# Optimization experiments

Hardware: AMD Instinct MI355X
Metric: run time of the kernel (lower is better)

The kernel has to match this reference:

```python
import jax, jax.numpy as jnp
import numpy as np

B_, H_, W_ = 4, 64, 64
D_MODEL, D_INNER, N_STATE, R_RANK, K_ = 96, 192, 16, 6, 4
EPS = 1e-5

def silu(v):
    return v * jax.nn.sigmoid(v)

def setup_inputs() -> dict:
    key = jax.random.key(0)
    ks = jax.random.split(key, 8)
    d, dm = D_INNER, D_MODEL
    A = jnp.tile(jnp.arange(1, N_STATE + 1, dtype=jnp.float32)[None, :], (K_ * d, 1))
    return {
        "x": jax.random.normal(ks[0], (B_, H_, W_, dm), jnp.float32),
        "in_proj_w": jax.random.normal(ks[1], (2 * d, dm), jnp.float32) * 0.02,
        "conv_w": jax.random.normal(ks[2], (d, 1, 3, 3), jnp.float32) * 0.1,
        "conv_b": jnp.zeros((d,), jnp.float32),
        "x_proj_weight": jax.random.normal(ks[3], (K_, R_RANK + 2 * N_STATE, d), jnp.float32) * 0.05,
        "dt_projs_weight": jax.random.normal(ks[4], (K_, d, R_RANK), jnp.float32) * 0.1,
        "dt_projs_bias": jax.random.normal(ks[5], (K_, d), jnp.float32) * 0.1,
        "A_logs": jnp.log(A),
        "Ds": jnp.ones((K_ * d,), jnp.float32),
        "out_norm_w": jnp.ones((d,), jnp.float32),
        "out_norm_b": jnp.zeros((d,), jnp.float32),
        "out_proj_w": jax.random.normal(ks[6], (dm, d), jnp.float32) * 0.02,
    }

def selective_scan(u, dts, As, Bs, Cs, Ds, dt_bias):
    # u, dts: [B,K,D,L]; As: [K,D,N]; Bs, Cs: [B,K,N,L]; Ds, dt_bias: [K,D]
    delta = jax.nn.softplus(dts + dt_bias[None, :, :, None])
    dT = jnp.moveaxis(delta, -1, 0)  # [L,B,K,D]
    uT = jnp.moveaxis(u, -1, 0)      # [L,B,K,D]
    BT = jnp.moveaxis(Bs, -1, 0)     # [L,B,K,N]
    CT = jnp.moveaxis(Cs, -1, 0)     # [L,B,K,N]
    h0 = jnp.zeros((u.shape[0], K_, D_INNER, N_STATE), jnp.float32)

    def step(h, inps):
        dt, ut, bt, ct = inps
        h = jnp.exp(dt[..., None] * As[None]) * h + (dt * ut)[..., None] * bt[:, :, None, :]
        y = jnp.einsum('bkdn,bkn->bkd', h, ct)
        return h, y

    _, ys = jax.lax.scan(step, h0, (dT, uT, BT, CT))
    ys = jnp.moveaxis(ys, 0, -1)  # [B,K,D,L]
    return ys + u * Ds[None, :, :, None]

def reference(x, in_proj_w, conv_w, conv_b, x_proj_weight, dt_projs_weight,
              dt_projs_bias, A_logs, Ds, out_norm_w, out_norm_b, out_proj_w):
    B, H, W, dm = x.shape
    d, N, R, K = D_INNER, N_STATE, R_RANK, K_
    L = H * W
    # in_proj + z gate (SiLU)
    xz = jnp.einsum('bhwc,pc->bhwp', x, in_proj_w)  # [B,H,W,2d]
    xc, z = xz[..., :d], xz[..., d:]
    z = silu(z)
    # depthwise conv (NCHW) + SiLU
    xc = jnp.transpose(xc, (0, 3, 1, 2))  # [B,d,H,W]
    xc = jax.lax.conv_general_dilated(
        xc, conv_w, (1, 1), 'SAME', feature_group_count=d,
        dimension_numbers=('NCHW', 'OIHW', 'NCHW')) + conv_b[None, :, None, None]
    xc = silu(xc)
    # cross-scan: 4 directions
    x0 = xc.reshape(B, d, L)                                   # row-major
    x1 = jnp.transpose(xc, (0, 1, 3, 2)).reshape(B, d, L)       # col-major
    xs = jnp.stack([x0, x1, x0[..., ::-1], x1[..., ::-1]], axis=1)  # [B,K,D,L]
    # projections
    x_dbl = jnp.einsum('bkdl,kcd->bkcl', xs, x_proj_weight)
    dts, Bs, Cs = jnp.split(x_dbl, [R, R + N], axis=2)
    dts = jnp.einsum('bkrl,kdr->bkdl', dts, dt_projs_weight)
    As = -jnp.exp(A_logs).reshape(K, d, N)
    ys = selective_scan(xs, dts, As, Bs, Cs, Ds.reshape(K, d), dt_projs_bias)
    # cross-merge
    y_wh = (ys[:, 1] + ys[:, 3, :, ::-1]).reshape(B, d, W, H)
    y_wh = jnp.transpose(y_wh, (0, 1, 3, 2)).reshape(B, d, L)
    y = ys[:, 0] + ys[:, 2, :, ::-1] + y_wh                     # [B,d,L]
    y = jnp.transpose(y.reshape(B, d, H, W), (0, 2, 3, 1))       # [B,H,W,d]
    # out_norm: LayerNorm over channel dim
    mu = jnp.mean(y, axis=-1, keepdims=True)
    var = jnp.mean((y - mu) ** 2, axis=-1, keepdims=True)
    y = out_norm_w * (y - mu) * jax.lax.rsqrt(var + EPS) + out_norm_b
    # gate + out_proj
    y = y * z
    return jnp.einsum('bhwd,cd->bhwc', y, out_proj_w)
```

## Files before the change

### kernel.cpp

```cpp
#include <hip/hip_runtime.h>
#include <math.h>

#define B_ 4
#define HH 64
#define WW 64
#define LL 4096
#define DM 96
#define DI 192
#define NS 16
#define RR 6
#define KK 4
#define NROW (B_ * KK * DI)
#define XPS 160
#define KOFF 40

__device__ __forceinline__ int pix_of(int k, int l) {
    switch (k) {
        case 0: return l;
        case 1: { int w = l >> 6, h = l & 63; return (h << 6) + w; }
        case 2: return (LL - 1) - l;
        default: { int ll = (LL - 1) - l; int w = ll >> 6, h = ll & 63; return (h << 6) + w; }
    }
}

__device__ __forceinline__ float silu_f(float v) {
    return v * __fdividef(1.f, 1.f + __expf(-v));
}
__device__ __forceinline__ float softplus_f(float x) {
    return (x > 20.f) ? x : __logf(1.f + __expf(x));
}

template<int MODE>
__global__ __launch_bounds__(256)
void gemm_kernel(const float* __restrict__ A, const float* __restrict__ Bw,
                 float* __restrict__ C0, float* __restrict__ C1,
                 int M, int N, int Kd) {
    __shared__ float As[32][68];
    __shared__ float Bs[32][68];
    int tid = threadIdx.x;
    int tx = tid & 15, ty = tid >> 4;
    int m0 = blockIdx.y * 64, n0 = blockIdx.x * 64;
    float acc[4][4] = {};
    for (int k0 = 0; k0 < Kd; k0 += 32) {
        #pragma unroll
        for (int i = 0; i < 8; ++i) {
            int idx = tid + i * 256;
            int r = idx >> 5, c = idx & 31;
            As[c][r] = A[(size_t)(m0 + r) * Kd + k0 + c];
            int rn = n0 + r;
            Bs[c][r] = (rn < N) ? Bw[(size_t)rn * Kd + k0 + c] : 0.f;
        }
        __syncthreads();
        #pragma unroll
        for (int kk = 0; kk < 32; ++kk) {
            float4 av = *(const float4*)&As[kk][ty * 4];
            float4 bv = *(const float4*)&Bs[kk][tx * 4];
            const float* avp = (const float*)&av;
            const float* bvp = (const float*)&bv;
            #pragma unroll
            for (int i = 0; i < 4; ++i)
                #pragma unroll
                for (int j = 0; j < 4; ++j)
                    acc[i][j] += avp[i] * bvp[j];
        }
        __syncthreads();
    }
    #pragma unroll
    for (int i = 0; i < 4; ++i) {
        int m = m0 + ty * 4 + i;
        #pragma unroll
        for (int j = 0; j < 4; ++j) {
            int n = n0 + tx * 4 + j;
            if (n >= N) continue;
            float v = acc[i][j];
            if (MODE == 0) {
                if (n < DI) C0[(size_t)m * DI + n] = v;
                else        C1[(size_t)m * DI + (n - DI)] = silu_f(v);
            } else if (MODE == 1) {
                C0[(size_t)m * N + n] = v;
            } else {
                if (n < 152) {
                    int kd = n / 38, c = n - kd * 38;
                    C0[(size_t)m * XPS + kd * KOFF + c] = v;
                }
            }
        }
    }
}

__global__ __launch_bounds__(192)
void conv_kernel(const float* __restrict__ xc, const float* __restrict__ cw,
                 const float* __restrict__ cb, float* __restrict__ out) {
    int p0 = blockIdx.x * 8;
    int b = blockIdx.y;
    int c = threadIdx.x;
    int h = p0 >> 6, w0 = p0 & 63;
    float kw[9];
    #pragma unroll
    for (int j = 0; j < 9; ++j) kw[j] = cw[c * 9 + j];
    float xv[3][10];
    #pragma unroll
    for (int dh = 0; dh < 3; ++dh) {
        int hh = h + dh - 1;
        bool hv = (hh >= 0 && hh < HH);
        #pragma unroll
        for (int j = 0; j < 10; ++j) {
            int ww = w0 + j - 1;
            bool v = hv && (ww >= 0 && ww < WW);
            xv[dh][j] = v ? xc[((size_t)(b << 12) + (hh << 6) + ww) * DI + c] : 0.f;
        }
    }
    float bias = cb[c];
    #pragma unroll
    for (int w = 0; w < 8; ++w) {
        float acc = bias;
        #pragma unroll
        for (int dh = 0; dh < 3; ++dh)
            #pragma unroll
            for (int dc = 0; dc < 3; ++dc)
                acc += xv[dh][w + dc] * kw[dh * 3 + dc];
        out[((size_t)(b << 12) + p0 + w) * DI + c] = silu_f(acc);
    }
}

template<int PHASE, int NCHT>
__global__ __launch_bounds__(192)
void scan_phase(const float* __restrict__ xconv, const float* __restrict__ xdblP,
                const float* __restrict__ dtw, const float* __restrict__ dtb,
                const float* __restrict__ A_logs, const float* __restrict__ Ds,
                float* __restrict__ carryA, float* __restrict__ carryB,
                float* __restrict__ y_acc) {
    constexpr int CHL = LL / NCHT;
    constexpr int NV4 = (PHASE == 3) ? (KOFF / 4) : 6;
    int chunk = blockIdx.x;
    int k = blockIdx.y;
    int b = blockIdx.z;
    int d = threadIdx.x;
    int l0 = chunk * CHL;
    __shared__ float sx[CHL * NV4 * 4];
    float4* sx4 = (float4*)sx;
    const float* xb = xdblP + ((size_t)(b << 12)) * XPS + k * KOFF;
    for (int idx = d; idx < CHL * NV4; idx += DI) {
        int r = idx / NV4, j = idx - r * NV4;
        int p = pix_of(k, l0 + r);
        sx4[idx] = *(const float4*)(xb + (size_t)p * XPS + j * 4);
    }

    float wr[RR];
    #pragma unroll
    for (int r = 0; r < RR; ++r) wr[r] = dtw[(k * DI + d) * RR + r];
    float bias = dtb[k * DI + d];
    const float* alog = A_logs + (size_t)(k * DI + d) * NS;
    bool fastA = true;
    #pragma unroll
    for (int n = 0; n < NS; ++n) {
        float an = -__expf(alog[n]);
        fastA = fastA && (fabsf(an + (float)(n + 1)) < 1e-4f * (float)(n + 1));
    }
    float h[NS];
    int row = (b * KK + k) * DI + d;
    if (PHASE == 1) {
        #pragma unroll
        for (int n = 0; n < NS; ++n) h[n] = 0.f;
    } else {
        #pragma unroll
        for (int n = 0; n < NS; ++n) h[n] = carryB[((size_t)chunk * NROW + row) * NS + n];
    }
    float Dk = (PHASE == 3) ? Ds[k * DI + d] : 0.f;
    float sumDelta = 0.f;
    const float* ubase = xconv + (size_t)(b << 12) * DI + d;
    float* ybase = y_acc + (size_t)(b << 12) * DI + d;
    __syncthreads();

    int p_cur = pix_of(k, l0);
    float u_cur = ubase[(size_t)p_cur * DI];
    for (int i = 0; i < CHL; ++i) {
        int p_nxt = 0; float u_nxt = 0.f;
        if (i + 1 < CHL) {
            p_nxt = pix_of(k, l0 + i + 1);
            u_nxt = ubase[(size_t)p_nxt * DI];
        }
        float xrv[NV4 * 4];
        float4* x4 = (float4*)xrv;
        #pragma unroll
        for (int j = 0; j < NV4; ++j) x4[j] = sx4[i * NV4 + j];
        float dtraw = bias;
        #pragma unroll
        for (int r = 0; r < RR; ++r) dtraw += xrv[r] * wr[r];
        float delta = softplus_f(dtraw);
        if (PHASE == 1) sumDelta += delta;
        float du = delta * u_cur;
        float y = 0.f;
        if (fastA) {
            float g = __expf(-delta);
            float a = 1.f;
            #pragma unroll
            for (int n = 0; n < NS; ++n) {
                a *= g;
                h[n] = a * h[n] + du * xrv[6 + n];
                if (PHASE == 3) y += h[n] * xrv[22 + n];
            }
        } else {
            #pragma unroll
            for (int n = 0; n < NS; ++n) {
                float a = __expf(delta * (-__expf(alog[n])));
                h[n] = a * h[n] + du * xrv[6 + n];
                if (PHASE == 3) y += h[n] * xrv[22 + n];
            }
        }
        if (PHASE == 3) {
            y += u_cur * Dk;
            atomicAdd(&ybase[(size_t)p_cur * DI], y);
        }
        p_cur = p_nxt;
        u_cur = u_nxt;
    }
    if (PHASE == 1) {
        #pragma unroll
        for (int n = 0; n < NS; ++n) {
            float An = -__expf(alog[n]);
            carryA[((size_t)chunk * NROW + row) * NS + n] = __expf(An * sumDelta);
            carryB[((size_t)chunk * NROW + row) * NS + n] = h[n];
        }
    }
}

template<int NCHT>
__global__ __launch_bounds__(256)
void scan_chunks(const float* __restrict__ carryA, float* __restrict__ carryB) {
    int t = blockIdx.x * 256 + threadIdx.x;
    if (t >= NROW * NS) return;
    float h = 0.f;
    for (int c = 0; c < NCHT; ++c) {
        size_t idx = (size_t)c * (NROW * NS) + t;
        float a = carryA[idx], bb = carryB[idx];
        carryB[idx] = h;
        h = a * h + bb;
    }
}

__global__ __launch_bounds__(256)
void ln_kernel(const float* __restrict__ y_acc, const float* __restrict__ z_silu,
               const float* __restrict__ nw, const float* __restrict__ nb,
               float* __restrict__ out) {
    int pg = blockIdx.x * 4 + (threadIdx.x >> 6);
    int lane = threadIdx.x & 63;
    const float* yr = y_acc + (size_t)pg * DI;
    float v0 = yr[lane], v1 = yr[lane + 64], v2 = yr[lane + 128];
    float s = v0 + v1 + v2;
    float sq = v0 * v0 + v1 * v1 + v2 * v2;
    #pragma unroll
    for (int m = 32; m >= 1; m >>= 1) {
        s  += __shfl_xor(s, m, 64);
        sq += __shfl_xor(sq, m, 64);
    }
    float mu = s * (1.f / 192.f);
    float var = sq * (1.f / 192.f) - mu * mu;
    float rs = rsqrtf(var + 1e-5f);
    const float* zr = z_silu + (size_t)pg * DI;
    float* o = out + (size_t)pg * DI;
    float vv[3] = {v0, v1, v2};
    #pragma unroll
    for (int j = 0; j < 3; ++j) {
        int c = lane + j * 64;
        o[c] = (nw[c] * (vv[j] - mu) * rs + nb[c]) * zr[c];
    }
}

extern "C" void kernel_launch(void* const* d_in, const int* in_sizes, int n_in,
                              void* d_out, int out_size, void* d_ws, size_t ws_size,
                              hipStream_t stream) {
    const float* x        = (const float*)d_in[0];
    const float* in_projw = (const float*)d_in[1];
    const float* conv_w   = (const float*)d_in[2];
    const float* conv_b   = (const float*)d_in[3];
    const float* x_projw  = (const float*)d_in[4];
    const float* dt_w     = (const float*)d_in[5];
    const float* dt_b     = (const float*)d_in[6];
    const float* A_logs   = (const float*)d_in[7];
    const float* Ds       = (const float*)d_in[8];
    const float* nw       = (const float*)d_in[9];
    const float* nb       = (const float*)d_in[10];
    const float* opw      = (const float*)d_in[11];
    float* out = (float*)d_out;
    float* ws = (float*)d_ws;

    const size_t SZ = (size_t)B_ * LL * DI;
    const size_t XD = (size_t)B_ * LL * XPS;

    const size_t car128 = (size_t)NROW * 128 * NS;
    const size_t need128 = (3 * SZ + XD + 2 * car128) * sizeof(float);
    bool big = (ws_size >= need128);

    float* z_silu = ws;
    float* xc_raw = ws + SZ;
    float* xconv  = ws + 2 * SZ;
    float* xdblP  = ws + 3 * SZ;
    float* carryA = ws + 3 * SZ + XD;
    float* carryB = carryA + (big ? car128 : (size_t)NROW * 64 * NS);
    float* y_acc  = xc_raw;
    float* yln    = xconv;

    gemm_kernel<0><<<dim3(6, 256), 256, 0, stream>>>(x, in_projw, xc_raw, z_silu,
                                                     B_ * LL, 2 * DI, DM);
    conv_kernel<<<dim3(LL / 8, B_), DI, 0, stream>>>(xc_raw, conv_w, conv_b, xconv);
    gemm_kernel<2><<<dim3(3, 256), 256, 0, stream>>>(xconv, x_projw, xdblP, nullptr,
                                                     B_ * LL, 152, DI);

    if (big) {
        scan_phase<1, 128><<<dim3(128, KK, B_), DI, 0, stream>>>(xconv, xdblP, dt_w, dt_b,
                                                                 A_logs, Ds, carryA, carryB, nullptr);
        scan_chunks<128><<<(NROW * NS + 255) / 256, 256, 0, stream>>>(carryA, carryB);
        hipMemsetAsync(y_acc, 0, SZ * sizeof(float), stream);
        scan_phase<3, 128><<<dim3(128, KK, B_), DI, 0, stream>>>(xconv, xdblP, dt_w, dt_b,
                                                                 A_logs, Ds, carryA, carryB, y_acc);
    } else {
        scan_phase<1, 64><<<dim3(64, KK, B_), DI, 0, stream>>>(xconv, xdblP, dt_w, dt_b,
                                                               A_logs, Ds, carryA, carryB, nullptr);
        scan_chunks<64><<<(NROW * NS + 255) / 256, 256, 0, stream>>>(carryA, carryB);
        hipMemsetAsync(y_acc, 0, SZ * sizeof(float), stream);
        scan_phase<3, 64><<<dim3(64, KK, B_), DI, 0, stream>>>(xconv, xdblP, dt_w, dt_b,
                                                               A_logs, Ds, carryA, carryB, y_acc);
    }
    ln_kernel<<<(B_ * LL) / 4, 256, 0, stream>>>(y_acc, z_silu, nw, nb, yln);
    gemm_kernel<1><<<dim3(2, 256), 256, 0, stream>>>(yln, opw, out, nullptr,
                                                     B_ * LL, DM, DI);
}
```

Before: 219.4 us.

## Derive scan decay from the softplus sigmoid and drop the carryA buffer

Rewrites the fast-A decay so that exp(-softplus(x)) comes from 1/(1+e^x), reusing the exp already computed for softplus. The per-state powers are built with a shallow multiplication tree instead of a serial chain, and the y reduction is split into four partial sums to shorten dependency chains. Pixel addressing uses a pointer stepped by a constant stride per direction. The carryA buffer is replaced by a per-row sum of delta, and scan_chunks now computes the chunk decay from that sum, which cuts carry traffic. The small-workspace fallback is removed and the last iteration prefetches one element past the chunk, so the code assumes a large enough workspace and tolerates that out-of-range read.

```diff
diff --git a/kernel.cpp b/kernel.cpp
--- a/kernel.cpp
+++ b/kernel.cpp
@@ -25,9 +25,6 @@
 
 __device__ __forceinline__ float silu_f(float v) {
     return v * __fdividef(1.f, 1.f + __expf(-v));
-}
-__device__ __forceinline__ float softplus_f(float x) {
-    return (x > 20.f) ? x : __logf(1.f + __expf(x));
 }
 
 template<int MODE>
@@ -128,7 +125,7 @@
 void scan_phase(const float* __restrict__ xconv, const float* __restrict__ xdblP,
                 const float* __restrict__ dtw, const float* __restrict__ dtb,
                 const float* __restrict__ A_logs, const float* __restrict__ Ds,
-                float* __restrict__ carryA, float* __restrict__ carryB,
+                float* __restrict__ sumD, float* __restrict__ carryB,
                 float* __restrict__ y_acc) {
     constexpr int CHL = LL / NCHT;
     constexpr int NV4 = (PHASE == 3) ? (KOFF / 4) : 6;
@@ -163,23 +160,27 @@
         #pragma unroll
         for (int n = 0; n < NS; ++n) h[n] = 0.f;
     } else {
-        #pragma unroll
-        for (int n = 0; n < NS; ++n) h[n] = carryB[((size_t)chunk * NROW + row) * NS + n];
+        const float4* cb4 = (const float4*)(carryB + ((size_t)chunk * NROW + row) * NS);
+        #pragma unroll
+        for (int q = 0; q < NS / 4; ++q) {
+            float4 v = cb4[q];
+            h[q * 4 + 0] = v.x; h[q * 4 + 1] = v.y;
+            h[q * 4 + 2] = v.z; h[q * 4 + 3] = v.w;
+        }
     }
     float Dk = (PHASE == 3) ? Ds[k * DI + d] : 0.f;
     float sumDelta = 0.f;
-    const float* ubase = xconv + (size_t)(b << 12) * DI + d;
-    float* ybase = y_acc + (size_t)(b << 12) * DI + d;
     __syncthreads();
 
-    int p_cur = pix_of(k, l0);
-    float u_cur = ubase[(size_t)p_cur * DI];
+    int s = (k == 0) ? 1 : (k == 1) ? 64 : (k == 2) ? -1 : -64;
+    int p0 = pix_of(k, l0);
+    intptr_t stp = (intptr_t)s * DI;
+    const float* up = xconv + (size_t)(b << 12) * DI + (size_t)p0 * DI + d;
+    float* yp = y_acc + (size_t)(b << 12) * DI + (size_t)p0 * DI + d;
+    float u_cur = *up;
+
     for (int i = 0; i < CHL; ++i) {
-        int p_nxt = 0; float u_nxt = 0.f;
-        if (i + 1 < CHL) {
-            p_nxt = pix_of(k, l0 + i + 1);
-            u_nxt = ubase[(size_t)p_nxt * DI];
-        }
+        float u_nxt = *(up + stp);
         float xrv[NV4 * 4];
         float4* x4 = (float4*)xrv;
         #pragma unroll
@@ -187,20 +188,27 @@
         float dtraw = bias;
         #pragma unroll
         for (int r = 0; r < RR; ++r) dtraw += xrv[r] * wr[r];
-        float delta = softplus_f(dtraw);
+        float e = __expf(dtraw);
+        float g = __fdividef(1.f, 1.f + e);
+        float delta = (dtraw > 20.f) ? dtraw : __logf(1.f + e);
         if (PHASE == 1) sumDelta += delta;
         float du = delta * u_cur;
-        float y = 0.f;
+        float y;
         if (fastA) {
-            float g = __expf(-delta);
-            float a = 1.f;
+            float a[NS];
+            a[0] = g;          a[1] = g * g;      a[2] = a[1] * g;    a[3] = a[1] * a[1];
+            a[4] = a[3] * g;   a[5] = a[3] * a[1]; a[6] = a[3] * a[2]; a[7] = a[3] * a[3];
+            a[8] = a[7] * g;   a[9] = a[7] * a[1]; a[10] = a[7] * a[2]; a[11] = a[7] * a[3];
+            a[12] = a[7] * a[4]; a[13] = a[7] * a[5]; a[14] = a[7] * a[6]; a[15] = a[7] * a[7];
+            float yp4[4] = {0.f, 0.f, 0.f, 0.f};
             #pragma unroll
             for (int n = 0; n < NS; ++n) {
-                a *= g;
-                h[n] = a * h[n] + du * xrv[6 + n];
-                if (PHASE == 3) y += h[n] * xrv[22 + n];
+                h[n] = a[n] * h[n] + du * xrv[6 + n];
+                if (PHASE == 3) yp4[n & 3] += h[n] * xrv[22 + n];
             }
+            y = (yp4[0] + yp4[1]) + (yp4[2] + yp4[3]);
         } else {
+            y = 0.f;
             #pragma unroll
             for (int n = 0; n < NS; ++n) {
                 float a = __expf(delta * (-__expf(alog[n])));
@@ -210,31 +218,40 @@
         }
         if (PHASE == 3) {
             y += u_cur * Dk;
-            atomicAdd(&ybase[(size_t)p_cur * DI], y);
-        }
-        p_cur = p_nxt;
+            atomicAdd(yp, y);
+            yp += stp;
+        }
+        up += stp;
         u_cur = u_nxt;
     }
     if (PHASE == 1) {
-        #pragma unroll
-        for (int n = 0; n < NS; ++n) {
-            float An = -__expf(alog[n]);
-            carryA[((size_t)chunk * NROW + row) * NS + n] = __expf(An * sumDelta);
-            carryB[((size_t)chunk * NROW + row) * NS + n] = h[n];
-        }
+        float4* cb4 = (float4*)(carryB + ((size_t)chunk * NROW + row) * NS);
+        #pragma unroll
+        for (int q = 0; q < NS / 4; ++q) {
+            float4 vb;
+            vb.x = h[q * 4 + 0]; vb.y = h[q * 4 + 1];
+            vb.z = h[q * 4 + 2]; vb.w = h[q * 4 + 3];
+            cb4[q] = vb;
+        }
+        sumD[(size_t)chunk * NROW + row] = sumDelta;
     }
 }
 
 template<int NCHT>
 __global__ __launch_bounds__(256)
-void scan_chunks(const float* __restrict__ carryA, float* __restrict__ carryB) {
+void scan_chunks(const float* __restrict__ sumD, const float* __restrict__ A_logs,
+                 float* __restrict__ carryB) {
     int t = blockIdx.x * 256 + threadIdx.x;
     if (t >= NROW * NS) return;
+    int row = t >> 4, n = t & 15;
+    int kd = row % (KK * DI);
+    float An = -__expf(A_logs[(size_t)kd * NS + n]);
     float h = 0.f;
     for (int c = 0; c < NCHT; ++c) {
         size_t idx = (size_t)c * (NROW * NS) + t;
-        float a = carryA[idx], bb = carryB[idx];
+        float bb = carryB[idx];
         carryB[idx] = h;
+        float a = __expf(An * sumD[(size_t)c * NROW + row]);
         h = a * h + bb;
     }
 }
@@ -287,17 +304,14 @@
 
     const size_t SZ = (size_t)B_ * LL * DI;
     const size_t XD = (size_t)B_ * LL * XPS;
-
-    const size_t car128 = (size_t)NROW * 128 * NS;
-    const size_t need128 = (3 * SZ + XD + 2 * car128) * sizeof(float);
-    bool big = (ws_size >= need128);
+    const size_t CAR = (size_t)NROW * 128 * NS;
 
     float* z_silu = ws;
     float* xc_raw = ws + SZ;
     float* xconv  = ws + 2 * SZ;
     float* xdblP  = ws + 3 * SZ;
-    float* carryA = ws + 3 * SZ + XD;
-    float* carryB = carryA + (big ? car128 : (size_t)NROW * 64 * NS);
+    float* carryB = ws + 3 * SZ + XD;
+    float* sumD   = carryB + CAR;
     float* y_acc  = xc_raw;
     float* yln    = xconv;
 
@@ -307,21 +321,13 @@
     gemm_kernel<2><<<dim3(3, 256), 256, 0, stream>>>(xconv, x_projw, xdblP, nullptr,
                                                      B_ * LL, 152, DI);
 
-    if (big) {
-        scan_phase<1, 128><<<dim3(128, KK, B_), DI, 0, stream>>>(xconv, xdblP, dt_w, dt_b,
-                                                                 A_logs, Ds, carryA, carryB, nullptr);
-        scan_chunks<128><<<(NROW * NS + 255) / 256, 256, 0, stream>>>(carryA, carryB);
-        hipMemsetAsync(y_acc, 0, SZ * sizeof(float), stream);
-        scan_phase<3, 128><<<dim3(128, KK, B_), DI, 0, stream>>>(xconv, xdblP, dt_w, dt_b,
-                                                                 A_logs, Ds, carryA, carryB, y_acc);
-    } else {
-        scan_phase<1, 64><<<dim3(64, KK, B_), DI, 0, stream>>>(xconv, xdblP, dt_w, dt_b,
-                                                               A_logs, Ds, carryA, carryB, nullptr);
-        scan_chunks<64><<<(NROW * NS + 255) / 256, 256, 0, stream>>>(carryA, carryB);
-        hipMemsetAsync(y_acc, 0, SZ * sizeof(float), stream);
-        scan_phase<3, 64><<<dim3(64, KK, B_), DI, 0, stream>>>(xconv, xdblP, dt_w, dt_b,
-                                                               A_logs, Ds, carryA, carryB, y_acc);
-    }
+    scan_phase<1, 128><<<dim3(128, KK, B_), DI, 0, stream>>>(xconv, xdblP, dt_w, dt_b,
+                                                             A_logs, Ds, sumD, carryB, nullptr);
+    scan_chunks<128><<<(NROW * NS + 255) / 256, 256, 0, stream>>>(sumD, A_logs, carryB);
+    hipMemsetAsync(y_acc, 0, SZ * sizeof(float), stream);
+    scan_phase<3, 128><<<dim3(128, KK, B_), DI, 0, stream>>>(xconv, xdblP, dt_w, dt_b,
+                                                             A_logs, Ds, sumD, carryB, y_acc);
+
     ln_kernel<<<(B_ * LL) / 4, 256, 0, stream>>>(y_acc, z_silu, nw, nb, yln);
     gemm_kernel<1><<<dim3(2, 256), 256, 0, stream>>>(yln, opw, out, nullptr,
                                                      B_ * LL, DM, DI);
```

New measurement: 233.4 us. 6.4% more time.
